# Kernel optimization log

Measured on AMD Instinct MI355X. Metric: run time of the kernel, lower is better.

The kernel has to match this reference:

```python
import jax, jax.numpy as jnp
import numpy as np

EMBED = 2048
HEADS = 16
HEAD_DIM = EMBED // HEADS
FF = 4 * EMBED
EPS = 1e-5


def gelu_tanh(x):
    c = jnp.sqrt(jnp.asarray(2.0 / jnp.pi, x.dtype))
    return 0.5 * x * (1.0 + jnp.tanh(c * (x + 0.044715 * x ** 3)))


def layernorm(x, scale, shift):
    mean = jnp.mean(x, axis=-1, keepdims=True)
    var = jnp.mean((x - mean) ** 2, axis=-1, keepdims=True)  # unbiased=False
    return scale * ((x - mean) / jnp.sqrt(var + EPS)) + shift


def setup_inputs() -> dict:
    key = jax.random.key(0)
    ks = jax.random.split(key, 10)
    s = 0.02  # GPT-style init scale keeps logits sane
    x = jax.random.normal(ks[0], (4, 2048, EMBED), dtype=jnp.float32)
    return {
        "x": x,
        "wq": jax.random.normal(ks[1], (EMBED, EMBED), jnp.float32) * s,
        "wk": jax.random.normal(ks[2], (EMBED, EMBED), jnp.float32) * s,
        "wv": jax.random.normal(ks[3], (EMBED, EMBED), jnp.float32) * s,
        "wo": jax.random.normal(ks[4], (EMBED, EMBED), jnp.float32) * s,
        "bo": jnp.zeros((EMBED,), jnp.float32),
        "w1": jax.random.normal(ks[5], (EMBED, FF), jnp.float32) * s,
        "b1": jnp.zeros((FF,), jnp.float32),
        "w2": jax.random.normal(ks[6], (FF, EMBED), jnp.float32) * s,
        "b2": jnp.zeros((EMBED,), jnp.float32),
        "ln1_scale": jnp.ones((EMBED,), jnp.float32),
        "ln1_shift": jnp.zeros((EMBED,), jnp.float32),
        "ln2_scale": jnp.ones((EMBED,), jnp.float32),
        "ln2_shift": jnp.zeros((EMBED,), jnp.float32),
    }


def reference(x, wq, wk, wv, wo, bo, w1, b1, w2, b2,
              ln1_scale, ln1_shift, ln2_scale, ln2_shift):
    b, s, d = x.shape
    # --- attention sub-block (pre-norm) ---
    h = layernorm(x, ln1_scale, ln1_shift)
    q = (h @ wq).reshape(b, s, HEADS, HEAD_DIM)
    k = (h @ wk).reshape(b, s, HEADS, HEAD_DIM)
    v = (h @ wv).reshape(b, s, HEADS, HEAD_DIM)
    scores = jnp.einsum("bqhd,bkhd->bhqk", q, k) / jnp.sqrt(
        jnp.asarray(HEAD_DIM, x.dtype))
    causal = jnp.triu(jnp.full((s, s), -jnp.inf, x.dtype), k=1)
    scores = scores + causal
    attn = jax.nn.softmax(scores, axis=-1)  # dropout p=0 -> identity
    ctx = jnp.einsum("bhqk,bkhd->bqhd", attn, v).reshape(b, s, d)
    x = x + (ctx @ wo + bo)
    # --- FFN sub-block (pre-norm) ---
    h = layernorm(x, ln2_scale, ln2_shift)
    h = gelu_tanh(h @ w1 + b1) @ w2 + b2
    return x + h
```

## Files before the change

### kernel.cpp

```cpp
#include <hip/hip_runtime.h>
#include <stdint.h>


#define EMBED 2048
#define SEQ   2048
#define BATCH 4
#define NROWS (BATCH*SEQ)
#define FFDIM 8192
#define HEADS 16
#define HD    128
#define QKS   4096

typedef unsigned short ushort_t;
typedef float f32x4 __attribute__((ext_vector_type(4)));
typedef short s16x8 __attribute__((ext_vector_type(8)));
typedef ushort_t u16x4 __attribute__((ext_vector_type(4)));

__device__ __forceinline__ ushort_t f2bf(float f) {
  unsigned u = __builtin_bit_cast(unsigned, f);
  u += 0x7fffu + ((u >> 16) & 1u);
  return (ushort_t)(u >> 16);
}
__device__ __forceinline__ float bf2f(ushort_t h) {
  unsigned u = ((unsigned)h) << 16;
  return __builtin_bit_cast(float, u);
}
__device__ __forceinline__ void split2(float f, ushort_t& hi, ushort_t& lo) {
  hi = f2bf(f);
  lo = f2bf(f - bf2f(hi));
}

#define MFMA16(a,b,c) __builtin_amdgcn_mfma_f32_16x16x32_bf16((a),(b),(c),0,0,0)

__device__ __forceinline__ void gload16(const void* g, void* l) {
  __builtin_amdgcn_global_load_lds((const __attribute__((address_space(1))) void*)g,
                                   (__attribute__((address_space(3))) void*)l,
                                   16, 0, 0);
}

__global__ __launch_bounds__(256)
void ln_split(const float* __restrict__ x, const float* __restrict__ sc,
              const float* __restrict__ sh, ushort_t* __restrict__ hi,
              ushort_t* __restrict__ lo)
{
  __shared__ float rs[4], rq[4];
  const int row = blockIdx.x, t = threadIdx.x;
  const int lane = t & 63, w = t >> 6;
  const float* xr = x + (size_t)row * EMBED;
  f32x4 a = *(const f32x4*)(xr + t*4);
  f32x4 b = *(const f32x4*)(xr + 1024 + t*4);
  float s = 0.f, q = 0.f;
  #pragma unroll
  for (int e=0;e<4;++e){ s += a[e]+b[e]; q += a[e]*a[e]+b[e]*b[e]; }
  #pragma unroll
  for (int m=1;m<64;m<<=1){ s += __shfl_xor(s,m,64); q += __shfl_xor(q,m,64); }
  if (lane==0){ rs[w]=s; rq[w]=q; }
  __syncthreads();
  s = rs[0]+rs[1]+rs[2]+rs[3];
  q = rq[0]+rq[1]+rq[2]+rq[3];
  const float mean = s * (1.f/EMBED);
  const float var  = fmaxf(q*(1.f/EMBED) - mean*mean, 0.f);
  const float rstd = rsqrtf(var + 1e-5f);
  #pragma unroll
  for (int half=0; half<2; ++half) {
    const int c0 = half*1024 + t*4;
    f32x4 v = half ? b : a;
    #pragma unroll
    for (int e=0;e<4;++e) {
      float o = sc[c0+e]*((v[e]-mean)*rstd) + sh[c0+e];
      ushort_t hh, ll; split2(o, hh, ll);
      hi[(size_t)row*EMBED + c0+e] = hh;
      lo[(size_t)row*EMBED + c0+e] = ll;
    }
  }
}

__global__ __launch_bounds__(256)
void wtrans_split(const float* __restrict__ W, int ldW, int K,
                  ushort_t* __restrict__ Thi, ushort_t* __restrict__ Tlo)
{
  __shared__ float tile[32][33];
  const int n0 = blockIdx.x*32, k0 = blockIdx.y*32;
  const int tx = threadIdx.x & 31, ty = threadIdx.x >> 5;
  #pragma unroll
  for (int i=0;i<4;++i)
    tile[ty + i*8][tx] = W[(size_t)(k0 + ty + i*8)*ldW + n0 + tx];
  __syncthreads();
  #pragma unroll
  for (int i=0;i<4;++i) {
    const int nl = ty + i*8;
    float v = tile[tx][nl];
    ushort_t h, l; split2(v, h, l);
    const size_t idx = (size_t)(n0 + nl)*K + k0 + tx;
    Thi[idx] = h; Tlo[idx] = l;
  }
}

template<int EPI>
__global__ __launch_bounds__(256, 2)
void gemm_split(const ushort_t* __restrict__ Ahi, const ushort_t* __restrict__ Alo,
                const ushort_t* __restrict__ Bhi, const ushort_t* __restrict__ Blo,
                int M, int N, int K,
                float* __restrict__ outf,
                ushort_t* __restrict__ ohi, ushort_t* __restrict__ olo,
                ushort_t* __restrict__ ohi2, ushort_t* __restrict__ olo2,
                const float* __restrict__ bias, const float* __restrict__ resid)
{
  __shared__ __align__(16) char lds[65536];
  const int t = threadIdx.x, lane = t & 63;
  const int wid = t >> 6;
  const int l15 = lane & 15, g = lane >> 4;
  const int row0 = blockIdx.x * 128, col0 = blockIdx.y * 128;
  const int wm = (wid >> 1) * 64, wn = (wid & 1) * 64;
  f32x4 acc[4][4] = {};

  auto STAGE = [&](int k0_, int bufoff_) {
    #pragma unroll
    for (int i=0;i<4;++i) {
      const int qq = i*256 + t;
      const unsigned o = (unsigned)qq*16u;
      const int r = o >> 7, sp = (o >> 4) & 7;
      const int sd = sp ^ (r & 7);
      const size_t koff = (size_t)k0_ + (sd & 3)*8;
      const ushort_t* srcA = ((sd<4)?Ahi:Alo) + (size_t)(row0+r)*K + koff;
      const ushort_t* srcB = ((sd<4)?Bhi:Blo) + (size_t)(col0+r)*K + koff;
      char* du = lds + bufoff_ + (o - (unsigned)lane*16u);
      gload16(srcA, du);
      gload16(srcB, du + 16384);
    }
  };

  STAGE(0, 0);
  __syncthreads();
  int cur = 0;
  for (int k0 = 0; k0 < K; k0 += 32) {
    const int nxt = cur ^ 1;
    if (k0 + 32 < K) STAGE(k0 + 32, nxt*32768);
    const char* abase = lds + cur*32768;
    const char* bbase = abase + 16384;
    s16x8 ah[4], al_[4], bh[4], bl[4];
    #pragma unroll
    for (int mf=0; mf<4; ++mf) {
      const int r = wm + mf*16 + l15;
      const char* rp = abase + r*128;
      ah[mf]  = *(const s16x8*)(rp + ((g ^ (r&7))*16));
      al_[mf] = *(const s16x8*)(rp + (((4|g) ^ (r&7))*16));
    }
    #pragma unroll
    for (int nf=0; nf<4; ++nf) {
      const int r = wn + nf*16 + l15;
      const char* rp = bbase + r*128;
      bh[nf] = *(const s16x8*)(rp + ((g ^ (r&7))*16));
      bl[nf] = *(const s16x8*)(rp + (((4|g) ^ (r&7))*16));
    }
    #pragma unroll
    for (int mf=0; mf<4; ++mf)
      #pragma unroll
      for (int nf=0; nf<4; ++nf) {
        f32x4 c = acc[mf][nf];
        c = MFMA16(ah[mf],  bh[nf], c);
        c = MFMA16(ah[mf],  bl[nf], c);
        c = MFMA16(al_[mf], bh[nf], c);
        acc[mf][nf] = c;
      }
    __syncthreads();
    cur = nxt;
  }

  #pragma unroll
  for (int mf=0; mf<4; ++mf) {
    const int rr = row0 + wm + mf*16 + g*4;
    #pragma unroll
    for (int nf=0; nf<4; ++nf) {
      const int cc = col0 + wn + nf*16 + l15;
      if constexpr (EPI == 5) {
        if (col0 < 4096) {
          #pragma unroll
          for (int j=0;j<4;++j) {
            ushort_t hh, ll; split2(acc[mf][nf][j], hh, ll);
            const size_t idx = (size_t)(rr+j)*QKS + cc;
            ohi[idx] = hh; olo[idx] = ll;
          }
        } else {
          const int dd = cc - 4096;
          u16x4 hv, lv;
          #pragma unroll
          for (int j=0;j<4;++j) {
            ushort_t hh, ll; split2(acc[mf][nf][j], hh, ll);
            hv[j] = hh; lv[j] = ll;
          }
          *(u16x4*)(ohi2 + (size_t)dd*SEQ + rr) = hv;
          *(u16x4*)(olo2 + (size_t)dd*SEQ + rr) = lv;
        }
      } else {
        #pragma unroll
        for (int j=0;j<4;++j) {
          const size_t idx = (size_t)(rr+j)*N + cc;
          float v = acc[mf][nf][j];
          if constexpr (EPI == 2) {
            outf[idx] = resid[idx] + v + bias[cc];
          } else if constexpr (EPI == 3) {
            float u = v + bias[cc];
            float gg = 0.5f*u*(1.0f + tanhf(0.7978845608028654f*(u + 0.044715f*u*u*u)));
            ushort_t hh, ll; split2(gg, hh, ll);
            ohi[idx]=hh; olo[idx]=ll;
          } else {
            outf[idx] = resid[idx] + v;
          }
        }
      }
    }
  }
}

__global__ __launch_bounds__(512)
void attn_fwd(const ushort_t* __restrict__ QKhi, const ushort_t* __restrict__ QKlo,
              const ushort_t* __restrict__ VThi, const ushort_t* __restrict__ VTlo,
              ushort_t* __restrict__ Chi, ushort_t* __restrict__ Clo)
{
  __shared__ __align__(16) char kv[65536];
  __shared__ __align__(16) float plds[8][16][68];
  const int qb = blockIdx.x, hh_ = blockIdx.y;
  const int t = threadIdx.x, lane = t & 63, w = t >> 6;
  const int l15 = lane & 15, g = lane >> 4;
  const int qrow = qb*128 + w*16 + l15;
  const size_t qbase = (size_t)qrow*QKS + hh_*HD;
  s16x8 qh[4], ql[4];
  #pragma unroll
  for (int ks=0; ks<4; ++ks) {
    qh[ks] = *(const s16x8*)(QKhi + qbase + ks*32 + g*8);
    ql[ks] = *(const s16x8*)(QKlo + qbase + ks*32 + g*8);
  }
  f32x4 ctx[8] = {};
  float ms[4], ls[4];
  #pragma unroll
  for (int j=0;j<4;++j){ ms[j] = -__builtin_inff(); ls[j] = 0.f; }
  const int ntiles = qb*2 + 2;
  const float scale = 0.08838834764831844f;
  for (int kt=0; kt<ntiles; ++kt) {
    {
      const size_t kbase = (size_t)(kt*64)*QKS + 2048 + hh_*HD;
      #pragma unroll
      for (int i=0;i<2;++i) {
        const int qq = i*512 + t;
        const unsigned o = (unsigned)qq*16u;
        const int r = o >> 8, sp = (o >> 4) & 15;
        const int sd = (sp & 8) | ((sp & 7) ^ (r & 7));
        char* du = kv + (o - (unsigned)lane*16u);
        gload16(QKhi + kbase + (size_t)r*QKS + sd*8, du);
        gload16(QKlo + kbase + (size_t)r*QKS + sd*8, du + 16384);
      }
      const size_t vbase = (size_t)hh_*HD*SEQ + (size_t)kt*64;
      #pragma unroll
      for (int i=0;i<2;++i) {
        const int qq = i*512 + t;
        const unsigned o = (unsigned)qq*16u;
        const int r = o >> 7, sp = (o >> 4) & 7;
        const int sd = sp ^ (r & 7);
        char* du = kv + 32768 + (o - (unsigned)lane*16u);
        gload16(VThi + vbase + (size_t)r*SEQ + sd*8, du);
        gload16(VTlo + vbase + (size_t)r*SEQ + sd*8, du + 16384);
      }
    }
    __syncthreads();
    f32x4 sc[4];
    #pragma unroll
    for (int nf=0; nf<4; ++nf) {
      f32x4 s = {};
      const int rB = nf*16 + l15;
      const char* rp = kv + rB*256;
      #pragma unroll
      for (int ks=0; ks<4; ++ks) {
        const int slot = ks*4 + g;
        const int ph = (slot & 8) | ((slot & 7) ^ (rB & 7));
        s16x8 kbh = *(const s16x8*)(rp + ph*16);
        s16x8 kbl = *(const s16x8*)(rp + 16384 + ph*16);
        s = MFMA16(qh[ks], kbh, s);
        s = MFMA16(qh[ks], kbl, s);
        s = MFMA16(ql[ks], kbh, s);
      }
      sc[nf] = s;
    }
    const int rowq = qb*128 + w*16 + g*4;
    #pragma unroll
    for (int nf=0; nf<4; ++nf) {
      const int col = kt*64 + nf*16 + l15;
      #pragma unroll
      for (int j=0;j<4;++j) {
        float v = sc[nf][j]*scale;
        sc[nf][j] = (col > rowq + j) ? -__builtin_inff() : v;
      }
    }
    float tm[4], al[4], mnu[4], ts[4];
    #pragma unroll
    for (int j=0;j<4;++j) {
      float m = fmaxf(fmaxf(sc[0][j], sc[1][j]), fmaxf(sc[2][j], sc[3][j]));
      #pragma unroll
      for (int d=1; d<16; d<<=1) m = fmaxf(m, __shfl_xor(m, d, 64));
      tm[j] = m;
    }
    #pragma unroll
    for (int j=0;j<4;++j) {
      const float mo = ms[j];
      const float mn = fmaxf(mo, tm[j]);
      const float mu = fmaxf(mn, -1e30f);
      al[j] = expf(mo - mu);
      mnu[j] = mu; ms[j] = mn; ts[j] = 0.f;
    }
    #pragma unroll
    for (int nf=0; nf<4; ++nf)
      #pragma unroll
      for (int j=0;j<4;++j) {
        float p = expf(sc[nf][j] - mnu[j]);
        sc[nf][j] = p;
        ts[j] += p;
      }
    #pragma unroll
    for (int j=0;j<4;++j) {
      #pragma unroll
      for (int d=1; d<16; d<<=1) ts[j] += __shfl_xor(ts[j], d, 64);
      ls[j] = ls[j]*al[j] + ts[j];
    }
    #pragma unroll
    for (int nf2=0; nf2<8; ++nf2)
      #pragma unroll
      for (int j=0;j<4;++j) ctx[nf2][j] *= al[j];
    #pragma unroll
    for (int nf=0; nf<4; ++nf)
      #pragma unroll
      for (int j=0;j<4;++j)
        plds[w][g*4+j][nf*16+l15] = sc[nf][j];
    asm volatile("s_waitcnt lgkmcnt(0)" ::: "memory");
    __builtin_amdgcn_sched_barrier(0);
    #pragma unroll
    for (int ks2=0; ks2<2; ++ks2) {
      const float* pr = &plds[w][l15][ks2*32 + g*8];
      f32x4 p0 = *(const f32x4*)pr;
      f32x4 p1 = *(const f32x4*)(pr + 4);
      s16x8 ph8, pl8;
      #pragma unroll
      for (int e=0;e<4;++e) {
        ushort_t h1_, l1_; split2(p0[e], h1_, l1_);
        ph8[e] = (short)h1_; pl8[e] = (short)l1_;
        ushort_t h2_, l2_; split2(p1[e], h2_, l2_);
        ph8[e+4] = (short)h2_; pl8[e+4] = (short)l2_;
      }
      #pragma unroll
      for (int nf2=0; nf2<8; ++nf2) {
        const int rV = nf2*16 + l15;
        const int ph_ = (ks2*4 + g) ^ (rV & 7);
        const char* vp = kv + 32768 + rV*128 + ph_*16;
        s16x8 vbh = *(const s16x8*)vp;
        s16x8 vbl = *(const s16x8*)(vp + 16384);
        ctx[nf2] = MFMA16(ph8, vbh, ctx[nf2]);
        ctx[nf2] = MFMA16(ph8, vbl, ctx[nf2]);
        ctx[nf2] = MFMA16(pl8, vbh, ctx[nf2]);
      }
    }
    __syncthreads();
  }
  float rl[4];
  #pragma unroll
  for (int j=0;j<4;++j) rl[j] = 1.f / ls[j];
  #pragma unroll
  for (int nf2=0; nf2<8; ++nf2) {
    #pragma unroll
    for (int j=0;j<4;++j) {
      float v = ctx[nf2][j]*rl[j];
      const size_t idx = (size_t)(qb*128 + w*16 + g*4 + j)*EMBED
                       + hh_*HD + nf2*16 + l15;
      ushort_t hh, ll; split2(v, hh, ll);
      Chi[idx] = hh; Clo[idx] = ll;
    }
  }
}

extern "C" void kernel_launch(void* const* d_in, const int* in_sizes, int n_in,
                              void* d_out, int out_size, void* d_ws, size_t ws_size,
                              hipStream_t stream)
{
  (void)in_sizes; (void)n_in; (void)out_size; (void)ws_size;
  const float* x    = (const float*)d_in[0];
  const float* wq   = (const float*)d_in[1];
  const float* wk   = (const float*)d_in[2];
  const float* wv   = (const float*)d_in[3];
  const float* wo   = (const float*)d_in[4];
  const float* bo   = (const float*)d_in[5];
  const float* w1   = (const float*)d_in[6];
  const float* b1   = (const float*)d_in[7];
  const float* w2   = (const float*)d_in[8];
  const float* b2   = (const float*)d_in[9];
  const float* ln1s = (const float*)d_in[10];
  const float* ln1h = (const float*)d_in[11];
  const float* ln2s = (const float*)d_in[12];
  const float* ln2h = (const float*)d_in[13];
  float* dout = (float*)d_out;

  char* ws = (char*)d_ws;
  const size_t MB = 1ull << 20;
  ushort_t* qkvT_hi = (ushort_t*)(ws +   0*MB);
  ushort_t* qkvT_lo = (ushort_t*)(ws +  24*MB);
  ushort_t* woT_hi  = (ushort_t*)(ws +  48*MB);
  ushort_t* woT_lo  = (ushort_t*)(ws +  56*MB);
  ushort_t* h1_hi   = (ushort_t*)(ws +  64*MB);
  ushort_t* h1_lo   = (ushort_t*)(ws +  96*MB);
  ushort_t* qk_hi   = (ushort_t*)(ws + 128*MB);
  ushort_t* qk_lo   = (ushort_t*)(ws + 144*MB);
  ushort_t* vt_hi   = (ushort_t*)(ws + 160*MB);
  ushort_t* vt_lo   = (ushort_t*)(ws + 168*MB);
  ushort_t* h2_hi   = (ushort_t*)(ws +   0*MB);
  ushort_t* h2_lo   = (ushort_t*)(ws +  32*MB);
  ushort_t* h3_hi   = (ushort_t*)(ws +  64*MB);
  ushort_t* h3_lo   = (ushort_t*)(ws +  96*MB);
  ushort_t* wT_hi   = (ushort_t*)(ws + 128*MB);
  ushort_t* wT_lo   = (ushort_t*)(ws + 136*MB);

  wtrans_split<<<dim3(64,64), 256, 0, stream>>>(wq, EMBED, EMBED, qkvT_hi,            qkvT_lo);
  wtrans_split<<<dim3(64,64), 256, 0, stream>>>(wk, EMBED, EMBED, qkvT_hi + 2048*2048, qkvT_lo + 2048*2048);
  wtrans_split<<<dim3(64,64), 256, 0, stream>>>(wv, EMBED, EMBED, qkvT_hi + 4096*2048, qkvT_lo + 4096*2048);
  wtrans_split<<<dim3(64,64), 256, 0, stream>>>(wo, EMBED, EMBED, woT_hi, woT_lo);
  ln_split<<<NROWS, 256, 0, stream>>>(x, ln1s, ln1h, h1_hi, h1_lo);

  for (int b = 0; b < BATCH; ++b) {
    const size_t so = (size_t)b * SEQ * EMBED;
    gemm_split<5><<<dim3(16,48), 256, 0, stream>>>(
        h1_hi + so, h1_lo + so, qkvT_hi, qkvT_lo,
        SEQ, 6144, EMBED, nullptr, qk_hi, qk_lo, vt_hi, vt_lo, nullptr, nullptr);
    attn_fwd<<<dim3(16,16), 512, 0, stream>>>(qk_hi, qk_lo, vt_hi, vt_lo,
                                              h1_hi + so, h1_lo + so);
  }

  gemm_split<2><<<dim3(64,16), 256, 0, stream>>>(
      h1_hi, h1_lo, woT_hi, woT_lo, NROWS, EMBED, EMBED,
      dout, nullptr, nullptr, nullptr, nullptr, bo, x);

  ln_split<<<NROWS, 256, 0, stream>>>(dout, ln2s, ln2h, h2_hi, h2_lo);

  for (int c = 0; c < 4; ++c) {
    wtrans_split<<<dim3(64,64), 256, 0, stream>>>(w1 + c*2048, FFDIM, EMBED,
                                                  wT_hi, wT_lo);
    gemm_split<3><<<dim3(64,16), 256, 0, stream>>>(
        h2_hi, h2_lo, wT_hi, wT_lo, NROWS, EMBED, EMBED,
        nullptr, h3_hi, h3_lo, nullptr, nullptr, b1 + c*2048, nullptr);
    wtrans_split<<<dim3(64,64), 256, 0, stream>>>(w2 + (size_t)c*2048*EMBED,
                                                  EMBED, 2048, wT_hi, wT_lo);
    if (c == 0)
      gemm_split<2><<<dim3(64,16), 256, 0, stream>>>(
          h3_hi, h3_lo, wT_hi, wT_lo, NROWS, EMBED, 2048,
          dout, nullptr, nullptr, nullptr, nullptr, b2, dout);
    else
      gemm_split<4><<<dim3(64,16), 256, 0, stream>>>(
          h3_hi, h3_lo, wT_hi, wT_lo, NROWS, EMBED, 2048,
          dout, nullptr, nullptr, nullptr, nullptr, nullptr, dout);
  }
}
```

Baseline: 3.477 ms.

## Enlarge GEMM tiles to 256x256 with 512 threads and fuse FFN weight transposes

The split-bf16 GEMM moves from 128x128 tiles with 4 waves to 256x256 tiles with 8 waves. Each wave now covers 128x64, and the LDS double buffer grows to 128KB. Per-stage global pointers are precomputed once instead of recomputed every K step. The w1 and w2 chunk transposes are merged into one launch writing separate buffers. The larger tiles are meant to raise operand reuse and cut LDS and global traffic per MFMA. The cost is fewer blocks: the QKV GEMM drops to 192 blocks. There is also heavy register pressure (128 accumulator registers) under launch_bounds(512,2), which may cause spills.

```diff
diff --git a/kernel.cpp b/kernel.cpp
--- a/kernel.cpp
+++ b/kernel.cpp
@@ -96,8 +96,35 @@
   }
 }
 
+__global__ __launch_bounds__(256)
+void wtrans2_split(const float* __restrict__ W1, int ldW1,
+                   const float* __restrict__ W2, int ldW2, int K,
+                   ushort_t* __restrict__ T1hi, ushort_t* __restrict__ T1lo,
+                   ushort_t* __restrict__ T2hi, ushort_t* __restrict__ T2lo)
+{
+  __shared__ float tile[32][33];
+  const float* W = blockIdx.z ? W2 : W1;
+  const int ldW = blockIdx.z ? ldW2 : ldW1;
+  ushort_t* Thi = blockIdx.z ? T2hi : T1hi;
+  ushort_t* Tlo = blockIdx.z ? T2lo : T1lo;
+  const int n0 = blockIdx.x*32, k0 = blockIdx.y*32;
+  const int tx = threadIdx.x & 31, ty = threadIdx.x >> 5;
+  #pragma unroll
+  for (int i=0;i<4;++i)
+    tile[ty + i*8][tx] = W[(size_t)(k0 + ty + i*8)*ldW + n0 + tx];
+  __syncthreads();
+  #pragma unroll
+  for (int i=0;i<4;++i) {
+    const int nl = ty + i*8;
+    float v = tile[tx][nl];
+    ushort_t h, l; split2(v, h, l);
+    const size_t idx = (size_t)(n0 + nl)*K + k0 + tx;
+    Thi[idx] = h; Tlo[idx] = l;
+  }
+}
+
 template<int EPI>
-__global__ __launch_bounds__(256, 2)
+__global__ __launch_bounds__(512, 2)
 void gemm_split(const ushort_t* __restrict__ Ahi, const ushort_t* __restrict__ Alo,
                 const ushort_t* __restrict__ Bhi, const ushort_t* __restrict__ Blo,
                 int M, int N, int K,
@@ -106,46 +133,46 @@
                 ushort_t* __restrict__ ohi2, ushort_t* __restrict__ olo2,
                 const float* __restrict__ bias, const float* __restrict__ resid)
 {
-  __shared__ __align__(16) char lds[65536];
+  __shared__ __align__(16) char lds[131072];
   const int t = threadIdx.x, lane = t & 63;
   const int wid = t >> 6;
   const int l15 = lane & 15, g = lane >> 4;
-  const int row0 = blockIdx.x * 128, col0 = blockIdx.y * 128;
-  const int wm = (wid >> 1) * 64, wn = (wid & 1) * 64;
-  f32x4 acc[4][4] = {};
-
-  auto STAGE = [&](int k0_, int bufoff_) {
+  const int row0 = blockIdx.x * 256, col0 = blockIdx.y * 256;
+  const int wm = (wid >> 2) * 128, wn = (wid & 3) * 64;
+
+  const ushort_t* pA[4]; const ushort_t* pB[4]; int duo[4];
+  #pragma unroll
+  for (int i=0;i<4;++i) {
+    const int qq = i*512 + t;
+    const unsigned o = (unsigned)qq*16u;
+    const int r = o >> 7, sp = (o >> 4) & 7;
+    const int sd = sp ^ (r & 7);
+    const size_t koff = (size_t)((sd & 3)*8);
+    pA[i] = ((sd<4)?Ahi:Alo) + (size_t)(row0+r)*K + koff;
+    pB[i] = ((sd<4)?Bhi:Blo) + (size_t)(col0+r)*K + koff;
+    duo[i] = i*8192 + wid*1024;
+  }
+  auto STAGE = [&](int bufoff_) {
     #pragma unroll
     for (int i=0;i<4;++i) {
-      const int qq = i*256 + t;
-      const unsigned o = (unsigned)qq*16u;
-      const int r = o >> 7, sp = (o >> 4) & 7;
-      const int sd = sp ^ (r & 7);
-      const size_t koff = (size_t)k0_ + (sd & 3)*8;
-      const ushort_t* srcA = ((sd<4)?Ahi:Alo) + (size_t)(row0+r)*K + koff;
-      const ushort_t* srcB = ((sd<4)?Bhi:Blo) + (size_t)(col0+r)*K + koff;
-      char* du = lds + bufoff_ + (o - (unsigned)lane*16u);
-      gload16(srcA, du);
-      gload16(srcB, du + 16384);
+      char* du = lds + bufoff_ + duo[i];
+      gload16(pA[i], du);
+      gload16(pB[i], du + 32768);
+      pA[i] += 32; pB[i] += 32;
     }
   };
 
-  STAGE(0, 0);
+  f32x4 acc[8][4] = {};
+  STAGE(0);
   __syncthreads();
   int cur = 0;
-  for (int k0 = 0; k0 < K; k0 += 32) {
+  const int nstep = K >> 5;
+  for (int ks = 0; ks < nstep; ++ks) {
     const int nxt = cur ^ 1;
-    if (k0 + 32 < K) STAGE(k0 + 32, nxt*32768);
-    const char* abase = lds + cur*32768;
-    const char* bbase = abase + 16384;
-    s16x8 ah[4], al_[4], bh[4], bl[4];
-    #pragma unroll
-    for (int mf=0; mf<4; ++mf) {
-      const int r = wm + mf*16 + l15;
-      const char* rp = abase + r*128;
-      ah[mf]  = *(const s16x8*)(rp + ((g ^ (r&7))*16));
-      al_[mf] = *(const s16x8*)(rp + (((4|g) ^ (r&7))*16));
-    }
+    if (ks + 1 < nstep) STAGE(nxt*65536);
+    const char* abase = lds + cur*65536;
+    const char* bbase = abase + 32768;
+    s16x8 bh[4], bl[4];
     #pragma unroll
     for (int nf=0; nf<4; ++nf) {
       const int r = wn + nf*16 + l15;
@@ -154,21 +181,26 @@
       bl[nf] = *(const s16x8*)(rp + (((4|g) ^ (r&7))*16));
     }
     #pragma unroll
-    for (int mf=0; mf<4; ++mf)
+    for (int mf=0; mf<8; ++mf) {
+      const int r = wm + mf*16 + l15;
+      const char* rp = abase + r*128;
+      s16x8 ah  = *(const s16x8*)(rp + ((g ^ (r&7))*16));
+      s16x8 al_ = *(const s16x8*)(rp + (((4|g) ^ (r&7))*16));
       #pragma unroll
       for (int nf=0; nf<4; ++nf) {
         f32x4 c = acc[mf][nf];
-        c = MFMA16(ah[mf],  bh[nf], c);
-        c = MFMA16(ah[mf],  bl[nf], c);
-        c = MFMA16(al_[mf], bh[nf], c);
+        c = MFMA16(ah,  bh[nf], c);
+        c = MFMA16(ah,  bl[nf], c);
+        c = MFMA16(al_, bh[nf], c);
         acc[mf][nf] = c;
       }
+    }
     __syncthreads();
     cur = nxt;
   }
 
   #pragma unroll
-  for (int mf=0; mf<4; ++mf) {
+  for (int mf=0; mf<8; ++mf) {
     const int rr = row0 + wm + mf*16 + g*4;
     #pragma unroll
     for (int nf=0; nf<4; ++nf) {
@@ -414,8 +446,10 @@
   ushort_t* h3_lo   = (ushort_t*)(ws +  96*MB);
   ushort_t* wT_hi   = (ushort_t*)(ws + 128*MB);
   ushort_t* wT_lo   = (ushort_t*)(ws + 136*MB);
-
-  wtrans_split<<<dim3(64,64), 256, 0, stream>>>(wq, EMBED, EMBED, qkvT_hi,            qkvT_lo);
+  ushort_t* w2T_hi  = (ushort_t*)(ws + 144*MB);
+  ushort_t* w2T_lo  = (ushort_t*)(ws + 152*MB);
+
+  wtrans_split<<<dim3(64,64), 256, 0, stream>>>(wq, EMBED, EMBED, qkvT_hi,             qkvT_lo);
   wtrans_split<<<dim3(64,64), 256, 0, stream>>>(wk, EMBED, EMBED, qkvT_hi + 2048*2048, qkvT_lo + 2048*2048);
   wtrans_split<<<dim3(64,64), 256, 0, stream>>>(wv, EMBED, EMBED, qkvT_hi + 4096*2048, qkvT_lo + 4096*2048);
   wtrans_split<<<dim3(64,64), 256, 0, stream>>>(wo, EMBED, EMBED, woT_hi, woT_lo);
@@ -423,34 +457,33 @@
 
   for (int b = 0; b < BATCH; ++b) {
     const size_t so = (size_t)b * SEQ * EMBED;
-    gemm_split<5><<<dim3(16,48), 256, 0, stream>>>(
+    gemm_split<5><<<dim3(8,24), 512, 0, stream>>>(
         h1_hi + so, h1_lo + so, qkvT_hi, qkvT_lo,
         SEQ, 6144, EMBED, nullptr, qk_hi, qk_lo, vt_hi, vt_lo, nullptr, nullptr);
     attn_fwd<<<dim3(16,16), 512, 0, stream>>>(qk_hi, qk_lo, vt_hi, vt_lo,
                                               h1_hi + so, h1_lo + so);
   }
 
-  gemm_split<2><<<dim3(64,16), 256, 0, stream>>>(
+  gemm_split<2><<<dim3(32,8), 512, 0, stream>>>(
       h1_hi, h1_lo, woT_hi, woT_lo, NROWS, EMBED, EMBED,
       dout, nullptr, nullptr, nullptr, nullptr, bo, x);
 
   ln_split<<<NROWS, 256, 0, stream>>>(dout, ln2s, ln2h, h2_hi, h2_lo);
 
   for (int c = 0; c < 4; ++c) {
-    wtrans_split<<<dim3(64,64), 256, 0, stream>>>(w1 + c*2048, FFDIM, EMBED,
-                                                  wT_hi, wT_lo);
-    gemm_split<3><<<dim3(64,16), 256, 0, stream>>>(
+    wtrans2_split<<<dim3(64,64,2), 256, 0, stream>>>(
+        w1 + c*2048, FFDIM, w2 + (size_t)c*2048*EMBED, EMBED, 2048,
+        wT_hi, wT_lo, w2T_hi, w2T_lo);
+    gemm_split<3><<<dim3(32,8), 512, 0, stream>>>(
         h2_hi, h2_lo, wT_hi, wT_lo, NROWS, EMBED, EMBED,
         nullptr, h3_hi, h3_lo, nullptr, nullptr, b1 + c*2048, nullptr);
-    wtrans_split<<<dim3(64,64), 256, 0, stream>>>(w2 + (size_t)c*2048*EMBED,
-                                                  EMBED, 2048, wT_hi, wT_lo);
     if (c == 0)
-      gemm_split<2><<<dim3(64,16), 256, 0, stream>>>(
-          h3_hi, h3_lo, wT_hi, wT_lo, NROWS, EMBED, 2048,
+      gemm_split<2><<<dim3(32,8), 512, 0, stream>>>(
+          h3_hi, h3_lo, w2T_hi, w2T_lo, NROWS, EMBED, 2048,
           dout, nullptr, nullptr, nullptr, nullptr, b2, dout);
     else
-      gemm_split<4><<<dim3(64,16), 256, 0, stream>>>(
-          h3_hi, h3_lo, wT_hi, wT_lo, NROWS, EMBED, 2048,
+      gemm_split<4><<<dim3(32,8), 512, 0, stream>>>(
+          h3_hi, h3_lo, w2T_hi, w2T_lo, NROWS, EMBED, 2048,
           dout, nullptr, nullptr, nullptr, nullptr, nullptr, dout);
   }
 }
```

Measured after the change: 3.025 ms. 13.0% less time.
